# Kernel tuning notes

Hardware: AMD Instinct MI355X
Metric: run time of the kernel (lower is better)

Reference implementation:

```python
import jax, jax.numpy as jnp
import numpy as np

DIM = 768
HEADS = 12
DH = DIM // HEADS
SCALE = DH ** -0.5


def setup_inputs() -> dict:
    key = jax.random.key(0)
    ks = jax.random.split(key, 8)
    B, N = 8, 1024
    x = jax.random.normal(ks[0], (B, N, DIM), dtype=jnp.float32)
    rpb = jax.random.normal(ks[1], (1, HEADS, N, N), dtype=jnp.float32)
    s = DIM ** -0.5
    W_qkv = jax.random.normal(ks[2], (DIM, 3 * DIM), dtype=jnp.float32) * s
    W_out = jax.random.normal(ks[3], (DIM, DIM), dtype=jnp.float32) * s
    b_out = jnp.zeros((DIM,), dtype=jnp.float32)
    ln_g = jnp.ones((DIM,), dtype=jnp.float32)
    ln_b = jnp.zeros((DIM,), dtype=jnp.float32)
    return {"x": x, "relative_position_bias": rpb, "W_qkv": W_qkv,
            "W_out": W_out, "b_out": b_out, "ln_g": ln_g, "ln_b": ln_b}


def reference(x, relative_position_bias, W_qkv, W_out, b_out, ln_g, ln_b):
    # LayerNorm (eps matches torch default 1e-5)
    mu = jnp.mean(x, axis=-1, keepdims=True)
    var = jnp.mean(jnp.square(x - mu), axis=-1, keepdims=True)
    xn = (x - mu) * jax.lax.rsqrt(var + 1e-5) * ln_g + ln_b

    qkv = xn @ W_qkv                                  # [b,n,3*dim]
    q, k, v = jnp.split(qkv, 3, axis=-1)
    B, N, _ = x.shape
    reshape = lambda t: t.reshape(B, N, HEADS, DH).transpose(0, 2, 1, 3)  # b h n d
    q, k, v = reshape(q), reshape(k), reshape(v)

    scores = jnp.einsum('bhid,bhjd->bhij', q, k) * SCALE + relative_position_bias
    attn = jax.nn.softmax(scores, axis=-1)            # dropout p=0.0 -> identity
    out = jnp.einsum('bhij,bhjd->bhid', attn, v)
    out = out.transpose(0, 2, 1, 3).reshape(B, N, HEADS * DH)
    return out @ W_out + b_out
```

## Files before the change

kernel.cpp:

```cpp
#include <hip/hip_runtime.h>
#include <hip/hip_bf16.h>
#include <math.h>

#define BATCH 8
#define NSEQ  1024
#define DIMM  768
#define NHEAD 12
#define DHEAD 64
#define SCALE 0.125f
#define ROWS  (BATCH * NSEQ)

typedef __hip_bfloat16 bf16;
typedef __bf16 bf16x8 __attribute__((ext_vector_type(8)));
typedef float  f32x4  __attribute__((ext_vector_type(4)));

#if __has_builtin(__builtin_amdgcn_global_load_lds)
#define HAVE_GLL 1
typedef __attribute__((address_space(3))) void lds_void_t;
typedef const __attribute__((address_space(1))) void gbl_void_t;
__device__ __forceinline__ void gload16(const void* g, void* l) {
    __builtin_amdgcn_global_load_lds((gbl_void_t*)g, (lds_void_t*)l, 16, 0, 0);
}
#else
#define HAVE_GLL 0
#endif

__device__ __forceinline__ unsigned pk2(float a, float b) {
    union { unsigned u; bf16 h[2]; } x;
    x.h[0] = __float2bfloat16(a);
    x.h[1] = __float2bfloat16(b);
    return x.u;
}

__global__ __launch_bounds__(256) void ln_kernel(const float* __restrict__ x,
                                                 const float* __restrict__ g,
                                                 const float* __restrict__ bta,
                                                 bf16* __restrict__ y) {
    __shared__ float ps[4], pq[4];
    __shared__ float mean_s, rstd_s;
    int row = blockIdx.x;
    int tid = threadIdx.x;
    const float* xr = x + (size_t)row * DIMM;
    float v[3];
    float s = 0.f, sq = 0.f;
#pragma unroll
    for (int i = 0; i < 3; ++i) {
        v[i] = xr[tid + 256 * i];
        s += v[i];
        sq += v[i] * v[i];
    }
#pragma unroll
    for (int off = 32; off >= 1; off >>= 1) {
        s  += __shfl_down(s, off);
        sq += __shfl_down(sq, off);
    }
    int wid = tid >> 6, lane = tid & 63;
    if (lane == 0) { ps[wid] = s; pq[wid] = sq; }
    __syncthreads();
    if (tid == 0) {
        float S = ps[0] + ps[1] + ps[2] + ps[3];
        float Q = pq[0] + pq[1] + pq[2] + pq[3];
        float mean = S * (1.0f / DIMM);
        float var  = Q * (1.0f / DIMM) - mean * mean;
        mean_s = mean;
        rstd_s = rsqrtf(fmaxf(var, 0.f) + 1e-5f);
    }
    __syncthreads();
    float mean = mean_s, rstd = rstd_s;
    bf16* yr = y + (size_t)row * DIMM;
#pragma unroll
    for (int i = 0; i < 3; ++i) {
        int c = tid + 256 * i;
        yr[c] = __float2bfloat16((v[i] - mean) * rstd * g[c] + bta[c]);
    }
}

__global__ __launch_bounds__(256) void transpose_bf16(const float* __restrict__ W,
                                                      bf16* __restrict__ Wt,
                                                      int K, int N) {
    __shared__ float t[32][33];
    int n0 = blockIdx.x * 32, k0 = blockIdx.y * 32;
    int tx = threadIdx.x, ty = threadIdx.y;
#pragma unroll
    for (int i = 0; i < 32; i += 8)
        t[ty + i][tx] = W[(size_t)(k0 + ty + i) * N + n0 + tx];
    __syncthreads();
#pragma unroll
    for (int i = 0; i < 32; i += 8)
        Wt[(size_t)(n0 + ty + i) * K + k0 + tx] = __float2bfloat16(t[tx][ty + i]);
}

template <bool OUT_BF16>
__global__ __launch_bounds__(256) void gemm_mfma(const bf16* __restrict__ A,
                                                 const bf16* __restrict__ Bt,
                                                 const float* __restrict__ bias,
                                                 void* __restrict__ Cv,
                                                 int M, int Nn, int K) {
    __shared__ bf16 As[128][32];
    __shared__ bf16 Bs[128][32];
    int tid = threadIdx.x;
    int wave = tid >> 6, lane = tid & 63, quad = lane >> 4, l16 = lane & 15;
    int wm = (wave >> 1) * 64, wn = (wave & 1) * 64;
    int m0 = blockIdx.y * 128, n0 = blockIdx.x * 128;

    f32x4 acc[4][4] = {};

#if HAVE_GLL
    const char* Ag = (const char*)(A  + (size_t)(m0 + (tid >> 2)) * K + (tid & 3) * 8);
    const char* Bg = (const char*)(Bt + (size_t)(n0 + (tid >> 2)) * K + (tid & 3) * 8);
    char* AsB = (char*)&As[0][0] + tid * 16;
    char* BsB = (char*)&Bs[0][0] + tid * 16;
    const size_t radv = (size_t)64 * K * 2;

    for (int k0 = 0; k0 < K; k0 += 32) {
        __syncthreads();
        gload16(Ag, AsB);
        gload16(Ag + radv, AsB + 4096);
        gload16(Bg, BsB);
        gload16(Bg + radv, BsB + 4096);
        Ag += 64; Bg += 64;
        __syncthreads();
#else
    int srow = tid >> 1;
    int sk = (tid & 1) * 16;
    const bf16* Ap = A  + (size_t)(m0 + srow) * K + sk;
    const bf16* Bp = Bt + (size_t)(n0 + srow) * K + sk;
    for (int k0 = 0; k0 < K; k0 += 32) {
        uint4 a0 = *(const uint4*)(Ap + k0);
        uint4 a1 = *(const uint4*)(Ap + k0 + 8);
        uint4 b0 = *(const uint4*)(Bp + k0);
        uint4 b1 = *(const uint4*)(Bp + k0 + 8);
        __syncthreads();
        *(uint4*)&As[srow][sk]     = a0;
        *(uint4*)&As[srow][sk + 8] = a1;
        *(uint4*)&Bs[srow][sk]     = b0;
        *(uint4*)&Bs[srow][sk + 8] = b1;
        __syncthreads();
#endif
        bf16x8 af[4], bf_[4];
#pragma unroll
        for (int i = 0; i < 4; ++i) {
            af[i]  = *(const bf16x8*)&As[wm + i * 16 + l16][quad * 8];
            bf_[i] = *(const bf16x8*)&Bs[wn + i * 16 + l16][quad * 8];
        }
#pragma unroll
        for (int mi = 0; mi < 4; ++mi)
#pragma unroll
            for (int ni = 0; ni < 4; ++ni)
                acc[mi][ni] = __builtin_amdgcn_mfma_f32_16x16x32_bf16(
                    af[mi], bf_[ni], acc[mi][ni], 0, 0, 0);
    }

    float bv[4] = {0.f, 0.f, 0.f, 0.f};
    if (!OUT_BF16 && bias) {
#pragma unroll
        for (int ni = 0; ni < 4; ++ni) bv[ni] = bias[n0 + wn + ni * 16 + l16];
    }
#pragma unroll
    for (int mi = 0; mi < 4; ++mi)
#pragma unroll
        for (int reg = 0; reg < 4; ++reg) {
            size_t row = m0 + wm + mi * 16 + quad * 4 + reg;
#pragma unroll
            for (int ni = 0; ni < 4; ++ni) {
                int col = n0 + wn + ni * 16 + l16;
                float val = acc[mi][ni][reg] + bv[ni];
                if (OUT_BF16)
                    ((bf16*)Cv)[row * Nn + col] = __float2bfloat16(val);
                else
                    ((float*)Cv)[row * Nn + col] = val;
            }
        }
}

#define KTILEB (64 * 3 * DIMM * 2)

__global__ __launch_bounds__(256, 4) void attn_mfma(const bf16* __restrict__ qkv,
                                                    const float* __restrict__ rpb,
                                                    bf16* __restrict__ outb) {
    __shared__ char KsRaw[2][8192];
    __shared__ unsigned Vt32[2][64][36];
    __shared__ bf16 Ps[4][16][72];

    int tid = threadIdx.x;
    int wave = tid >> 6, lane = tid & 63, quad = lane >> 4, l16 = lane & 15;
    int bid = blockIdx.x;
    int b  = bid & 7;
    int r2 = bid >> 3;
    int h  = r2 % NHEAD;
    int mt = r2 / NHEAD;
    int m0 = mt * 64;

    const bf16* qrow = qkv + (size_t)(b * NSEQ + m0 + wave * 16 + l16) * (3 * DIMM) + h * DHEAD;
    bf16x8 qf0 = *(const bf16x8*)(qrow + quad * 8);
    bf16x8 qf1 = *(const bf16x8*)(qrow + 32 + quad * 8);

    const float* rp = rpb + ((size_t)h * NSEQ + (m0 + wave * 16 + l16)) * NSEQ;

#if HAVE_GLL
    const char* kgl = (const char*)(qkv + (size_t)(b * NSEQ + wave * 16 + l16) * (3 * DIMM)
                                    + DIMM + h * DHEAD + quad * 8);
    char* kdst = &KsRaw[0][0] + tid * 16 + wave * 1024;
#else
    int ksr = tid >> 2, ksd = (tid & 3) * 16;
    const bf16* kgf = qkv + (size_t)(b * NSEQ + ksr) * (3 * DIMM) + DIMM + h * DHEAD + ksd;
#endif

    int vk = (tid >> 3) * 2;
    int vd = (tid & 7) * 8;
    int vkp = tid >> 3;
    const bf16* vg = qkv + (size_t)(b * NSEQ + vk) * (3 * DIMM) + 2 * DIMM + h * DHEAD + vd;
    int wblk = (((vkp >> 2) ^ (vd >> 3)) << 2) | (vkp & 3);

    float m_s = -INFINITY, l_s = 0.f;
    f32x4 acco[4] = {};

#if HAVE_GLL
    gload16(kgl, kdst);
    gload16(kgl + 64, kdst + 1024);
#endif
    uint4 va = *(const uint4*)(vg);
    uint4 vb = *(const uint4*)(vg + 3 * DIMM);
#if !HAVE_GLL
    {
        uint4 k0v = *(const uint4*)(kgf);
        uint4 k1v = *(const uint4*)(kgf + 8);
        bf16* kb = (bf16*)(&KsRaw[0][0] + (ksr >> 4) * 2048 + ((ksr & 15)) * 16);
        char* d0 = &KsRaw[0][0] + (ksr >> 4) * 2048 + (ksd >> 5) * 1024 + ((((ksd >> 3) & 3) * 16 + (ksr & 15)) * 16);
        *(uint4*)d0 = k0v;
        char* d1 = &KsRaw[0][0] + (ksr >> 4) * 2048 + ((ksd + 8) >> 5) * 1024 + (((((ksd + 8) >> 3) & 3) * 16 + (ksr & 15)) * 16);
        *(uint4*)d1 = k1v;
        (void)kb;
    }
#endif
    {
        union { uint4 q; unsigned short u[8]; } A_, B_;
        A_.q = va; B_.q = vb;
#pragma unroll
        for (int j = 0; j < 8; ++j)
            Vt32[0][vd + j][wblk] = (unsigned)A_.u[j] | ((unsigned)B_.u[j] << 16);
    }
    __syncthreads();

    for (int kt = 0; kt < 16; ++kt) {
        int cur = kt & 1, nxt = cur ^ 1;

        if (kt + 1 < 16) {
#if HAVE_GLL
            const char* kg2 = kgl + (size_t)(kt + 1) * KTILEB;
            gload16(kg2, kdst + nxt * 8192);
            gload16(kg2 + 64, kdst + nxt * 8192 + 1024);
#endif
            const bf16* v2 = vg + (size_t)(kt + 1) * 64 * (3 * DIMM);
            va = *(const uint4*)(v2);
            vb = *(const uint4*)(v2 + 3 * DIMM);
        }

        float4 rv[4];
        const float* rpk = rp + kt * 64;
#pragma unroll
        for (int t = 0; t < 4; ++t)
            rv[t] = *(const float4*)&rpk[t * 16 + quad * 4];

        f32x4 accs[4] = {};
#pragma unroll
        for (int t = 0; t < 4; ++t) {
            const char* kb = &KsRaw[cur][0] + t * 2048 + (quad * 16 + l16) * 16;
            bf16x8 kf0 = *(const bf16x8*)(kb);
            bf16x8 kf1 = *(const bf16x8*)(kb + 1024);
            accs[t] = __builtin_amdgcn_mfma_f32_16x16x32_bf16(kf0, qf0, accs[t], 0, 0, 0);
            accs[t] = __builtin_amdgcn_mfma_f32_16x16x32_bf16(kf1, qf1, accs[t], 0, 0, 0);
        }

        float mx = -INFINITY;
        {
            float rb[4][4] = {{rv[0].x, rv[0].y, rv[0].z, rv[0].w},
                              {rv[1].x, rv[1].y, rv[1].z, rv[1].w},
                              {rv[2].x, rv[2].y, rv[2].z, rv[2].w},
                              {rv[3].x, rv[3].y, rv[3].z, rv[3].w}};
#pragma unroll
            for (int t = 0; t < 4; ++t)
#pragma unroll
                for (int r = 0; r < 4; ++r) {
                    accs[t][r] = fmaf(accs[t][r], SCALE, rb[t][r]);
                    mx = fmaxf(mx, accs[t][r]);
                }
        }
        mx = fmaxf(mx, __shfl_xor(mx, 16));
        mx = fmaxf(mx, __shfl_xor(mx, 32));
        float mn = fmaxf(m_s, mx);
        float alpha = __expf(m_s - mn);
        m_s = mn;
        float sum = 0.f;
#pragma unroll
        for (int t = 0; t < 4; ++t)
#pragma unroll
            for (int r = 0; r < 4; ++r) {
                float p = __expf(accs[t][r] - mn);
                accs[t][r] = p;
                sum += p;
            }
        sum += __shfl_xor(sum, 16);
        sum += __shfl_xor(sum, 32);
        l_s = l_s * alpha + sum;

        float ab[4];
#pragma unroll
        for (int r = 0; r < 4; ++r) ab[r] = __shfl(alpha, quad * 4 + r);
#pragma unroll
        for (int dt = 0; dt < 4; ++dt)
#pragma unroll
            for (int r = 0; r < 4; ++r) acco[dt][r] *= ab[r];

#pragma unroll
        for (int t = 0; t < 4; ++t) {
            uint2 w;
            w.x = pk2(accs[t][0], accs[t][1]);
            w.y = pk2(accs[t][2], accs[t][3]);
            *(uint2*)&Ps[wave][l16][t * 16 + quad * 4] = w;
        }
        __asm__ volatile("s_waitcnt lgkmcnt(0)" ::: "memory");

#pragma unroll
        for (int s = 0; s < 2; ++s) {
            bf16x8 pf = *(const bf16x8*)&Ps[wave][l16][s * 32 + quad * 8];
#pragma unroll
            for (int dt = 0; dt < 4; ++dt) {
                int row = dt * 16 + l16;
                int sblk = (((s * 4 + quad) ^ ((row >> 3) & 7)) << 2);
                bf16x8 vf = *(const bf16x8*)&Vt32[cur][row][sblk];
                acco[dt] = __builtin_amdgcn_mfma_f32_16x16x32_bf16(pf, vf, acco[dt], 0, 0, 0);
            }
        }

        if (kt + 1 < 16) {
            union { uint4 q; unsigned short u[8]; } A_, B_;
            A_.q = va; B_.q = vb;
#pragma unroll
            for (int j = 0; j < 8; ++j)
                Vt32[nxt][vd + j][wblk] = (unsigned)A_.u[j] | ((unsigned)B_.u[j] << 16);
        }
        __syncthreads();
    }

    float invl[4];
#pragma unroll
    for (int r = 0; r < 4; ++r) invl[r] = 1.f / __shfl(l_s, quad * 4 + r);
    bf16* orow = outb + (size_t)(b * NSEQ + m0 + wave * 16) * DIMM + h * DHEAD;
#pragma unroll
    for (int dt = 0; dt < 4; ++dt)
#pragma unroll
        for (int r = 0; r < 4; ++r)
            orow[(size_t)(quad * 4 + r) * DIMM + dt * 16 + l16] =
                __float2bfloat16(acco[dt][r] * invl[r]);
}

extern "C" void kernel_launch(void* const* d_in, const int* in_sizes, int n_in,
                              void* d_out, int out_size, void* d_ws, size_t ws_size,
                              hipStream_t stream) {
    const float* x     = (const float*)d_in[0];
    const float* rpb   = (const float*)d_in[1];
    const float* W_qkv = (const float*)d_in[2];
    const float* W_out = (const float*)d_in[3];
    const float* b_out = (const float*)d_in[4];
    const float* ln_g  = (const float*)d_in[5];
    const float* ln_b  = (const float*)d_in[6];
    float* out = (float*)d_out;

    char* p = (char*)d_ws;
    bf16* xn    = (bf16*)p; p += (size_t)ROWS * DIMM * 2;
    bf16* qkv   = (bf16*)p; p += (size_t)ROWS * 3 * DIMM * 2;
    bf16* attn  = (bf16*)p; p += (size_t)ROWS * DIMM * 2;
    bf16* WqkvT = (bf16*)p; p += (size_t)3 * DIMM * DIMM * 2;
    bf16* WoutT = (bf16*)p; p += (size_t)DIMM * DIMM * 2;

    ln_kernel<<<ROWS, 256, 0, stream>>>(x, ln_g, ln_b, xn);
    transpose_bf16<<<dim3(3 * DIMM / 32, DIMM / 32), dim3(32, 8), 0, stream>>>(
        W_qkv, WqkvT, DIMM, 3 * DIMM);
    transpose_bf16<<<dim3(DIMM / 32, DIMM / 32), dim3(32, 8), 0, stream>>>(
        W_out, WoutT, DIMM, DIMM);

    gemm_mfma<true><<<dim3(3 * DIMM / 128, ROWS / 128), 256, 0, stream>>>(
        xn, WqkvT, nullptr, qkv, ROWS, 3 * DIMM, DIMM);

    attn_mfma<<<BATCH * NHEAD * (NSEQ / 64), 256, 0, stream>>>(qkv, rpb, attn);

    gemm_mfma<false><<<dim3(DIMM / 128, ROWS / 128), 256, 0, stream>>>(
        attn, WoutT, b_out, out, ROWS, DIMM, DIMM);
}
```

Baseline: 279.5 us.

## Use 128-row query blocks with 8 waves splitting K/V staging

Attention blocks now cover 128 query rows with 512 threads, so each K/V tile loaded into LDS serves twice as many queries and global K/V traffic is halved. Half the threads stage K via LDS DMA and the other half stage the transposed V. The block index is remapped so neighbouring blocks spread across the grid, and MFMA sections get raised wave priority through s_setprio. The price is fewer, larger blocks and launch bounds that may constrain registers.

```diff
diff --git a/kernel.cpp b/kernel.cpp
--- a/kernel.cpp
+++ b/kernel.cpp
@@ -174,22 +174,26 @@
 }
 
 #define KTILEB (64 * 3 * DIMM * 2)
-
-__global__ __launch_bounds__(256, 4) void attn_mfma(const bf16* __restrict__ qkv,
+#define QBLK   128
+#define NBLK   (BATCH * NHEAD * (NSEQ / QBLK))
+
+__global__ __launch_bounds__(512, 6) void attn_mfma(const bf16* __restrict__ qkv,
                                                     const float* __restrict__ rpb,
                                                     bf16* __restrict__ outb) {
     __shared__ char KsRaw[2][8192];
     __shared__ unsigned Vt32[2][64][36];
-    __shared__ bf16 Ps[4][16][72];
+    __shared__ bf16 Ps[8][16][72];
 
     int tid = threadIdx.x;
     int wave = tid >> 6, lane = tid & 63, quad = lane >> 4, l16 = lane & 15;
-    int bid = blockIdx.x;
-    int b  = bid & 7;
-    int r2 = bid >> 3;
+
+    int p  = blockIdx.x;
+    int wid = (p & 7) * (NBLK / 8) + (p >> 3);
+    int b  = wid & 7;
+    int r2 = wid >> 3;
     int h  = r2 % NHEAD;
     int mt = r2 / NHEAD;
-    int m0 = mt * 64;
+    int m0 = mt * QBLK;
 
     const bf16* qrow = qkv + (size_t)(b * NSEQ + m0 + wave * 16 + l16) * (3 * DIMM) + h * DHEAD;
     bf16x8 qf0 = *(const bf16x8*)(qrow + quad * 8);
@@ -197,43 +201,46 @@
 
     const float* rp = rpb + ((size_t)h * NSEQ + (m0 + wave * 16 + l16)) * NSEQ;
 
+    bool isK = (tid < 256);
+    int t2 = tid & 255;
+
 #if HAVE_GLL
-    const char* kgl = (const char*)(qkv + (size_t)(b * NSEQ + wave * 16 + l16) * (3 * DIMM)
+    const char* kgl = (const char*)(qkv + (size_t)(b * NSEQ + (t2 >> 6) * 16 + l16) * (3 * DIMM)
                                     + DIMM + h * DHEAD + quad * 8);
-    char* kdst = &KsRaw[0][0] + tid * 16 + wave * 1024;
+    char* kdst = &KsRaw[0][0] + t2 * 16 + (t2 >> 6) * 1024;
 #else
-    int ksr = tid >> 2, ksd = (tid & 3) * 16;
+    int ksr = t2 >> 2, ksd = (t2 & 3) * 16;
     const bf16* kgf = qkv + (size_t)(b * NSEQ + ksr) * (3 * DIMM) + DIMM + h * DHEAD + ksd;
 #endif
 
-    int vk = (tid >> 3) * 2;
-    int vd = (tid & 7) * 8;
-    int vkp = tid >> 3;
+    int vk = (t2 >> 3) * 2;
+    int vd = (t2 & 7) * 8;
+    int vkp = t2 >> 3;
     const bf16* vg = qkv + (size_t)(b * NSEQ + vk) * (3 * DIMM) + 2 * DIMM + h * DHEAD + vd;
     int wblk = (((vkp >> 2) ^ (vd >> 3)) << 2) | (vkp & 3);
 
     float m_s = -INFINITY, l_s = 0.f;
     f32x4 acco[4] = {};
 
+    uint4 va = {}, vb = {};
 #if HAVE_GLL
-    gload16(kgl, kdst);
-    gload16(kgl + 64, kdst + 1024);
-#endif
-    uint4 va = *(const uint4*)(vg);
-    uint4 vb = *(const uint4*)(vg + 3 * DIMM);
-#if !HAVE_GLL
-    {
+    if (isK) {
+        gload16(kgl, kdst);
+        gload16(kgl + 64, kdst + 1024);
+    }
+#else
+    if (isK) {
         uint4 k0v = *(const uint4*)(kgf);
         uint4 k1v = *(const uint4*)(kgf + 8);
-        bf16* kb = (bf16*)(&KsRaw[0][0] + (ksr >> 4) * 2048 + ((ksr & 15)) * 16);
         char* d0 = &KsRaw[0][0] + (ksr >> 4) * 2048 + (ksd >> 5) * 1024 + ((((ksd >> 3) & 3) * 16 + (ksr & 15)) * 16);
         *(uint4*)d0 = k0v;
         char* d1 = &KsRaw[0][0] + (ksr >> 4) * 2048 + ((ksd + 8) >> 5) * 1024 + (((((ksd + 8) >> 3) & 3) * 16 + (ksr & 15)) * 16);
         *(uint4*)d1 = k1v;
-        (void)kb;
     }
 #endif
-    {
+    if (!isK) {
+        va = *(const uint4*)(vg);
+        vb = *(const uint4*)(vg + 3 * DIMM);
         union { uint4 q; unsigned short u[8]; } A_, B_;
         A_.q = va; B_.q = vb;
 #pragma unroll
@@ -247,13 +254,17 @@
 
         if (kt + 1 < 16) {
 #if HAVE_GLL
-            const char* kg2 = kgl + (size_t)(kt + 1) * KTILEB;
-            gload16(kg2, kdst + nxt * 8192);
-            gload16(kg2 + 64, kdst + nxt * 8192 + 1024);
+            if (isK) {
+                const char* kg2 = kgl + (size_t)(kt + 1) * KTILEB;
+                gload16(kg2, kdst + nxt * 8192);
+                gload16(kg2 + 64, kdst + nxt * 8192 + 1024);
+            }
 #endif
-            const bf16* v2 = vg + (size_t)(kt + 1) * 64 * (3 * DIMM);
-            va = *(const uint4*)(v2);
-            vb = *(const uint4*)(v2 + 3 * DIMM);
+            if (!isK) {
+                const bf16* v2 = vg + (size_t)(kt + 1) * 64 * (3 * DIMM);
+                va = *(const uint4*)(v2);
+                vb = *(const uint4*)(v2 + 3 * DIMM);
+            }
         }
 
         float4 rv[4];
@@ -263,6 +274,7 @@
             rv[t] = *(const float4*)&rpk[t * 16 + quad * 4];
 
         f32x4 accs[4] = {};
+        __builtin_amdgcn_s_setprio(1);
 #pragma unroll
         for (int t = 0; t < 4; ++t) {
             const char* kb = &KsRaw[cur][0] + t * 2048 + (quad * 16 + l16) * 16;
@@ -271,6 +283,7 @@
             accs[t] = __builtin_amdgcn_mfma_f32_16x16x32_bf16(kf0, qf0, accs[t], 0, 0, 0);
             accs[t] = __builtin_amdgcn_mfma_f32_16x16x32_bf16(kf1, qf1, accs[t], 0, 0, 0);
         }
+        __builtin_amdgcn_s_setprio(0);
 
         float mx = -INFINITY;
         {
@@ -296,9 +309,9 @@
         for (int t = 0; t < 4; ++t)
 #pragma unroll
             for (int r = 0; r < 4; ++r) {
-                float p = __expf(accs[t][r] - mn);
-                accs[t][r] = p;
-                sum += p;
+                float pv = __expf(accs[t][r] - mn);
+                accs[t][r] = pv;
+                sum += pv;
             }
         sum += __shfl_xor(sum, 16);
         sum += __shfl_xor(sum, 32);
@@ -321,6 +334,7 @@
         }
         __asm__ volatile("s_waitcnt lgkmcnt(0)" ::: "memory");
 
+        __builtin_amdgcn_s_setprio(1);
 #pragma unroll
         for (int s = 0; s < 2; ++s) {
             bf16x8 pf = *(const bf16x8*)&Ps[wave][l16][s * 32 + quad * 8];
@@ -332,8 +346,9 @@
                 acco[dt] = __builtin_amdgcn_mfma_f32_16x16x32_bf16(pf, vf, acco[dt], 0, 0, 0);
             }
         }
-
-        if (kt + 1 < 16) {
+        __builtin_amdgcn_s_setprio(0);
+
+        if (!isK && kt + 1 < 16) {
             union { uint4 q; unsigned short u[8]; } A_, B_;
             A_.q = va; B_.q = vb;
 #pragma unroll
@@ -383,7 +398,7 @@
     gemm_mfma<true><<<dim3(3 * DIMM / 128, ROWS / 128), 256, 0, stream>>>(
         xn, WqkvT, nullptr, qkv, ROWS, 3 * DIMM, DIMM);
 
-    attn_mfma<<<BATCH * NHEAD * (NSEQ / 64), 256, 0, stream>>>(qkv, rpb, attn);
+    attn_mfma<<<NBLK, 512, 0, stream>>>(qkv, rpb, attn);
 
     gemm_mfma<false><<<dim3(DIMM / 128, ROWS / 128), 256, 0, stream>>>(
         attn, WoutT, b_out, out, ROWS, DIMM, DIMM);
```

Result: slower. 325.4 us (+16.4%).
